# Optimization experiments

Measured on AMD Instinct MI355X. Metric: run time of the kernel, lower is better.

Reference implementation:

```python
import jax, jax.numpy as jnp
import numpy as np

N, T, D = 128, 2048, 88

def setup_inputs() -> dict:
    key = jax.random.key(0)
    k1, k2 = jax.random.split(key)
    output = jax.random.normal(k1, (N, T, D), dtype=jnp.float32)
    # binary piano-roll style target (sparse note activations)
    target = (jax.random.uniform(k2, (N, T, D)) < 0.1).astype(jnp.float32)
    mask = jnp.ones((N, T), dtype=jnp.int32)  # left-aligned valid mask
    return {"output": output, "target": target, "mask": mask}

def reference(output, target, mask):
    # prediction = (sigmoid(output) > 0.5) -> non-differentiable 0/1 floats
    pred = (jax.nn.sigmoid(output) > 0.5).astype(output.dtype)
    # tru_pos summed over both feature and time dims -> [N]
    tru_pos = jnp.sum(pred * target, axis=(1, 2))
    # per-timestep false pos / false neg -> [N, T]
    false_pos = jnp.sum(pred * (1.0 - target), axis=2)
    false_neg = jnp.sum((1.0 - pred) * target, axis=2)
    # T_i = number of valid timesteps per sequence (loop runs over t < T_i)
    T_i = jnp.sum(mask, axis=1)  # [N] int
    valid = (jnp.arange(false_pos.shape[1])[None, :] < T_i[:, None]).astype(output.dtype)
    ratio = tru_pos[:, None] / (tru_pos[:, None] + false_pos + false_neg)  # [N, T]
    acc = jnp.sum(ratio * valid, axis=1) / T_i.astype(output.dtype)  # [N]
    return jnp.sum(acc)
```

## Files before the change

### kernel.cpp

```cpp
#include <hip/hip_runtime.h>

#define NN 128
#define TT 2048
#define DD 88
#define BLOCKS_PER_N 32
#define ROWS_PER_BLOCK (TT / BLOCKS_PER_N)

__global__ __launch_bounds__(256) void acc_rowstats_kernel(
    const float* __restrict__ out, const float* __restrict__ tgt,
    float* __restrict__ fpfn, float* __restrict__ tp_part) {
  const int blk = blockIdx.x;
  const int n = blk / BLOCKS_PER_N;
  const int chunk = blk % BLOCKS_PER_N;
  const int t0 = chunk * ROWS_PER_BLOCK;
  const int lane = threadIdx.x & 63;
  const int wave = threadIdx.x >> 6;

  float tp_acc = 0.f;
  for (int r = wave; r < ROWS_PER_BLOCK; r += 4) {
    const int t = t0 + r;
    const size_t base = ((size_t)n * TT + t) * DD;
    float fpfn_l = 0.f, tp_l = 0.f;
    {
      const float o = out[base + lane];
      const float g = tgt[base + lane];
      const bool p = o > 0.f;
      const bool gg = g > 0.5f;
      tp_l += (p && gg) ? 1.f : 0.f;
      fpfn_l += (p != gg) ? 1.f : 0.f;
    }
    if (lane < (DD - 64)) {
      const float o = out[base + 64 + lane];
      const float g = tgt[base + 64 + lane];
      const bool p = o > 0.f;
      const bool gg = g > 0.5f;
      tp_l += (p && gg) ? 1.f : 0.f;
      fpfn_l += (p != gg) ? 1.f : 0.f;
    }
    for (int off = 32; off > 0; off >>= 1)
      fpfn_l += __shfl_down(fpfn_l, off, 64);
    if (lane == 0) fpfn[(size_t)n * TT + t] = fpfn_l;
    tp_acc += tp_l;
  }
  for (int off = 32; off > 0; off >>= 1)
    tp_acc += __shfl_down(tp_acc, off, 64);
  __shared__ float s_tp[4];
  if (lane == 0) s_tp[wave] = tp_acc;
  __syncthreads();
  if (threadIdx.x == 0)
    tp_part[blk] = s_tp[0] + s_tp[1] + s_tp[2] + s_tp[3];
}

__global__ __launch_bounds__(256) void acc_finalize_kernel(
    const int* __restrict__ mask, const float* __restrict__ fpfn,
    const float* __restrict__ tp_part, float* __restrict__ out) {
  const int n = blockIdx.x;
  const int tid = threadIdx.x;
  __shared__ float sred[256];
  __shared__ float s_tp, s_ti;

  int ti = 0;
  for (int t = tid; t < TT; t += 256) ti += mask[n * TT + t];
  sred[tid] = (float)ti;
  __syncthreads();
  for (int s = 128; s > 0; s >>= 1) {
    if (tid < s) sred[tid] += sred[tid + s];
    __syncthreads();
  }
  if (tid == 0) s_ti = sred[0];
  __syncthreads();

  float tpv = (tid < BLOCKS_PER_N) ? tp_part[n * BLOCKS_PER_N + tid] : 0.f;
  sred[tid] = tpv;
  __syncthreads();
  for (int s = 128; s > 0; s >>= 1) {
    if (tid < s) sred[tid] += sred[tid + s];
    __syncthreads();
  }
  if (tid == 0) s_tp = sred[0];
  __syncthreads();

  const float tp = s_tp;
  const int Ti = (int)s_ti;

  float acc = 0.f;
  for (int t = tid; t < Ti; t += 256) {
    const float denom = tp + fpfn[(size_t)n * TT + t];
    acc += tp / denom;
  }
  sred[tid] = acc;
  __syncthreads();
  for (int s = 128; s > 0; s >>= 1) {
    if (tid < s) sred[tid] += sred[tid + s];
    __syncthreads();
  }
  if (tid == 0) atomicAdd(out, sred[0] / s_ti);
}

extern "C" void kernel_launch(void* const* d_in, const int* in_sizes, int n_in,
                              void* d_out, int out_size, void* d_ws, size_t ws_size,
                              hipStream_t stream) {
  const float* output = (const float*)d_in[0];
  const float* target = (const float*)d_in[1];
  const int* mask = (const int*)d_in[2];
  float* out = (float*)d_out;

  float* tp_part = (float*)d_ws;
  float* fpfn = tp_part + NN * BLOCKS_PER_N;

  hipMemsetAsync(d_out, 0, sizeof(float) * out_size, stream);

  acc_rowstats_kernel<<<NN * BLOCKS_PER_N, 256, 0, stream>>>(output, target, fpfn, tp_part);
  acc_finalize_kernel<<<NN, 256, 0, stream>>>(mask, fpfn, tp_part, out);
}
```

Measured before the change: 215.6 us.

## Vectorize row-stats loads with float4 tiles and LDS row reduction

The row-stats kernel now has each block process a contiguous 128-row tile. Each thread loads float4 vectors of output and target, computes false-positive plus false-negative partials arithmetically, and reduces per-row sums through LDS rather than a per-row wave shuffle reduction. This replaces scalar partially-masked loads with fully coalesced 16-byte loads and removes the per-row shuffle chains. The finalize kernel also vectorizes the mask read and combines the two reductions. The new code assumes the target is exactly 0 or 1, which holds because target is a binary mask.

```diff
diff --git a/kernel.cpp b/kernel.cpp
--- a/kernel.cpp
+++ b/kernel.cpp
@@ -3,52 +3,68 @@
 #define NN 128
 #define TT 2048
 #define DD 88
-#define BLOCKS_PER_N 32
-#define ROWS_PER_BLOCK (TT / BLOCKS_PER_N)
+#define ROWS_PER_BLK 128
+#define F4_PER_ROW 22
+#define F4_PER_TILE (ROWS_PER_BLK * F4_PER_ROW)
+#define K1_BLOCKS (NN * TT / ROWS_PER_BLK)
 
 __global__ __launch_bounds__(256) void acc_rowstats_kernel(
     const float* __restrict__ out, const float* __restrict__ tgt,
     float* __restrict__ fpfn, float* __restrict__ tp_part) {
+  __shared__ float lds_x[F4_PER_TILE];
+  const int tid = threadIdx.x;
   const int blk = blockIdx.x;
-  const int n = blk / BLOCKS_PER_N;
-  const int chunk = blk % BLOCKS_PER_N;
-  const int t0 = chunk * ROWS_PER_BLOCK;
-  const int lane = threadIdx.x & 63;
-  const int wave = threadIdx.x >> 6;
+  const size_t tile_f4 = (size_t)blk * F4_PER_TILE;
+  const float4* __restrict__ o4 = (const float4*)out;
+  const float4* __restrict__ g4 = (const float4*)tgt;
 
-  float tp_acc = 0.f;
-  for (int r = wave; r < ROWS_PER_BLOCK; r += 4) {
-    const int t = t0 + r;
-    const size_t base = ((size_t)n * TT + t) * DD;
-    float fpfn_l = 0.f, tp_l = 0.f;
+  float tp = 0.f;
+#pragma unroll
+  for (int it = 0; it < 11; ++it) {
+    const int f = it * 256 + tid;
+    const float4 o = o4[tile_f4 + f];
+    const float4 g = g4[tile_f4 + f];
+    float x = 0.f;
     {
-      const float o = out[base + lane];
-      const float g = tgt[base + lane];
-      const bool p = o > 0.f;
-      const bool gg = g > 0.5f;
-      tp_l += (p && gg) ? 1.f : 0.f;
-      fpfn_l += (p != gg) ? 1.f : 0.f;
+      const float pf = (o.x > 0.f) ? 1.f : 0.f;
+      x += fabsf(pf - g.x);
+      tp = fmaf(pf, g.x, tp);
     }
-    if (lane < (DD - 64)) {
-      const float o = out[base + 64 + lane];
-      const float g = tgt[base + 64 + lane];
-      const bool p = o > 0.f;
-      const bool gg = g > 0.5f;
-      tp_l += (p && gg) ? 1.f : 0.f;
-      fpfn_l += (p != gg) ? 1.f : 0.f;
+    {
+      const float pf = (o.y > 0.f) ? 1.f : 0.f;
+      x += fabsf(pf - g.y);
+      tp = fmaf(pf, g.y, tp);
     }
-    for (int off = 32; off > 0; off >>= 1)
-      fpfn_l += __shfl_down(fpfn_l, off, 64);
-    if (lane == 0) fpfn[(size_t)n * TT + t] = fpfn_l;
-    tp_acc += tp_l;
+    {
+      const float pf = (o.z > 0.f) ? 1.f : 0.f;
+      x += fabsf(pf - g.z);
+      tp = fmaf(pf, g.z, tp);
+    }
+    {
+      const float pf = (o.w > 0.f) ? 1.f : 0.f;
+      x += fabsf(pf - g.w);
+      tp = fmaf(pf, g.w, tp);
+    }
+    lds_x[f] = x;
   }
-  for (int off = 32; off > 0; off >>= 1)
-    tp_acc += __shfl_down(tp_acc, off, 64);
+  __syncthreads();
+
+  {
+    const int r = tid >> 1;
+    const int s = tid & 1;
+    float v = 0.f;
+#pragma unroll
+    for (int i = 0; i < 11; ++i) v += lds_x[r * F4_PER_ROW + s * 11 + i];
+    v += __shfl_down(v, 1, 64);
+    if (s == 0) fpfn[(size_t)blk * ROWS_PER_BLK + r] = v;
+  }
+
+  for (int off = 32; off > 0; off >>= 1) tp += __shfl_down(tp, off, 64);
   __shared__ float s_tp[4];
-  if (lane == 0) s_tp[wave] = tp_acc;
+  const int lane = tid & 63, wave = tid >> 6;
+  if (lane == 0) s_tp[wave] = tp;
   __syncthreads();
-  if (threadIdx.x == 0)
-    tp_part[blk] = s_tp[0] + s_tp[1] + s_tp[2] + s_tp[3];
+  if (tid == 0) tp_part[blk] = s_tp[0] + s_tp[1] + s_tp[2] + s_tp[3];
 }
 
 __global__ __launch_bounds__(256) void acc_finalize_kernel(
@@ -56,45 +72,39 @@
     const float* __restrict__ tp_part, float* __restrict__ out) {
   const int n = blockIdx.x;
   const int tid = threadIdx.x;
-  __shared__ float sred[256];
-  __shared__ float s_tp, s_ti;
+  __shared__ float sa[256], sb[256];
 
+  const int4* m4 = (const int4*)(mask + (size_t)n * TT);
   int ti = 0;
-  for (int t = tid; t < TT; t += 256) ti += mask[n * TT + t];
-  sred[tid] = (float)ti;
+#pragma unroll
+  for (int it = 0; it < 2; ++it) {
+    const int4 v = m4[it * 256 + tid];
+    ti += v.x + v.y + v.z + v.w;
+  }
+  const float tpv = (tid < 16) ? tp_part[n * 16 + tid] : 0.f;
+
+  sa[tid] = (float)ti;
+  sb[tid] = tpv;
   __syncthreads();
   for (int s = 128; s > 0; s >>= 1) {
-    if (tid < s) sred[tid] += sred[tid + s];
+    if (tid < s) { sa[tid] += sa[tid + s]; sb[tid] += sb[tid + s]; }
     __syncthreads();
   }
-  if (tid == 0) s_ti = sred[0];
+  const float fTi = sa[0];
+  const float tp = sb[0];
+  const int Ti = (int)fTi;
   __syncthreads();
 
-  float tpv = (tid < BLOCKS_PER_N) ? tp_part[n * BLOCKS_PER_N + tid] : 0.f;
-  sred[tid] = tpv;
+  const float* __restrict__ fr = fpfn + (size_t)n * TT;
+  float acc = 0.f;
+  for (int t = tid; t < Ti; t += 256) acc += tp / (tp + fr[t]);
+  sa[tid] = acc;
   __syncthreads();
   for (int s = 128; s > 0; s >>= 1) {
-    if (tid < s) sred[tid] += sred[tid + s];
+    if (tid < s) sa[tid] += sa[tid + s];
     __syncthreads();
   }
-  if (tid == 0) s_tp = sred[0];
-  __syncthreads();
-
-  const float tp = s_tp;
-  const int Ti = (int)s_ti;
-
-  float acc = 0.f;
-  for (int t = tid; t < Ti; t += 256) {
-    const float denom = tp + fpfn[(size_t)n * TT + t];
-    acc += tp / denom;
-  }
-  sred[tid] = acc;
-  __syncthreads();
-  for (int s = 128; s > 0; s >>= 1) {
-    if (tid < s) sred[tid] += sred[tid + s];
-    __syncthreads();
-  }
-  if (tid == 0) atomicAdd(out, sred[0] / s_ti);
+  if (tid == 0) atomicAdd(out, sa[0] / fTi);
 }
 
 extern "C" void kernel_launch(void* const* d_in, const int* in_sizes, int n_in,
@@ -106,10 +116,9 @@
   float* out = (float*)d_out;
 
   float* tp_part = (float*)d_ws;
-  float* fpfn = tp_part + NN * BLOCKS_PER_N;
+  float* fpfn = tp_part + K1_BLOCKS;
 
   hipMemsetAsync(d_out, 0, sizeof(float) * out_size, stream);
-
-  acc_rowstats_kernel<<<NN * BLOCKS_PER_N, 256, 0, stream>>>(output, target, fpfn, tp_part);
+  acc_rowstats_kernel<<<K1_BLOCKS, 256, 0, stream>>>(output, target, fpfn, tp_part);
   acc_finalize_kernel<<<NN, 256, 0, stream>>>(mask, fpfn, tp_part, out);
 }
```

Result: faster. 208.3 us (-3.4%).
